# Performance work log

Hardware: AMD Instinct MI355X
Metric: run time of the kernel (lower is better)

Reference implementation:

```python
import jax, jax.numpy as jnp
import numpy as np

N_HEAD = 12
N_EMBD = 768

def setup_inputs() -> dict:
    key = jax.random.key(0)
    k1, k2, k3 = jax.random.split(key, 3)
    B, T, C = 4, 2048, N_EMBD
    x = jax.random.normal(k1, (B, T, C), dtype=jnp.float32)
    w_attn = jax.random.normal(k2, (C, 3 * C), dtype=jnp.float32) * (C ** -0.5)
    b_attn = jnp.zeros((3 * C,), dtype=jnp.float32)
    w_proj = jax.random.normal(k3, (C, C), dtype=jnp.float32) * (C ** -0.5)
    b_proj = jnp.zeros((C,), dtype=jnp.float32)
    return {"x": x, "w_attn": w_attn, "b_attn": b_attn, "w_proj": w_proj, "b_proj": b_proj}

def reference(x, w_attn, b_attn, w_proj, b_proj):
    B, T, C = x.shape
    H = N_HEAD
    D = C // H
    qkv = x @ w_attn + b_attn  # [B,T,3C]
    q, k, v = jnp.split(qkv, 3, axis=-1)
    # [B,H,T,D]
    q = q.reshape(B, T, H, D).transpose(0, 2, 1, 3)
    k = k.reshape(B, T, H, D).transpose(0, 2, 1, 3)
    v = v.reshape(B, T, H, D).transpose(0, 2, 1, 3)
    # NOTE: source scales by n_embd**-0.5, not head_dim**-0.5
    scores = jnp.einsum('bhqd,bhkd->bhqk', q, k) * (C ** -0.5)
    causal = jnp.triu(jnp.ones((T, T), dtype=bool), k=1)  # True above diagonal
    scores = jnp.where(causal, -jnp.inf, scores)
    attn = jax.nn.softmax(scores, axis=-1)
    out = jnp.einsum('bhqk,bhkd->bhqd', attn, v)  # [B,H,T,D]
    out = out.transpose(0, 2, 1, 3).reshape(B, T, C)
    return out @ w_proj + b_proj
```

## Files before the change

### kernel.cpp

```cpp
#include <hip/hip_runtime.h>
#include <cstdint>
#include <cstddef>

typedef __attribute__((ext_vector_type(8))) short bf8_t;
typedef __attribute__((ext_vector_type(4))) float f4_t;
typedef __attribute__((ext_vector_type(16))) float f16v_t;
typedef __attribute__((ext_vector_type(2))) unsigned u2_t;
typedef __attribute__((ext_vector_type(4))) unsigned u4_t;

#define DEVFN static __device__ __forceinline__
#define MFMA16(a, b, c) __builtin_amdgcn_mfma_f32_16x16x32_bf16(a, b, c, 0, 0, 0)
#define MFMA32(a, b, c) __builtin_amdgcn_mfma_f32_32x32x16_bf16(a, b, c, 0, 0, 0)

constexpr float kQscale = 0.05205877317700523f;

DEVFN short f2bs(float f) {
  uint32_t u = __builtin_bit_cast(uint32_t, f);
  u = (u + 0x7FFFu + ((u >> 16) & 1u)) >> 16;
  return (short)(uint16_t)u;
}

DEVFN unsigned cvtpk(float lo, float hi) {
  unsigned r;
  asm("v_cvt_pk_bf16_f32 %0, %1, %2" : "=v"(r) : "v"(lo), "v"(hi));
  return r;
}

DEVFN float red2_sum(float v) { return v + __shfl_xor(v, 32, 64); }

DEVFN void gload16(const void* g, void* l) {
  __builtin_amdgcn_global_load_lds(
      (const __attribute__((address_space(1))) void*)g,
      (__attribute__((address_space(3))) void*)l, 16, 0, 0);
}

__global__ __launch_bounds__(256) void prep(const float* __restrict__ x,
                                            short* __restrict__ xb,
                                            const float* __restrict__ w_attn,
                                            short* __restrict__ wat,
                                            const float* __restrict__ w_proj,
                                            short* __restrict__ wpt) {
  __shared__ float tile[32][33];
  const int blk = blockIdx.x, tid = threadIdx.x;
  if (blk < 3072) {
    const int i = blk * 256 + tid;
    const f4_t* p = (const f4_t*)x + (size_t)i * 2;
    f4_t a = p[0], b = p[1];
    bf8_t h;
    h[0] = f2bs(a[0]); h[1] = f2bs(a[1]); h[2] = f2bs(a[2]); h[3] = f2bs(a[3]);
    h[4] = f2bs(b[0]); h[5] = f2bs(b[1]); h[6] = f2bs(b[2]); h[7] = f2bs(b[3]);
    *((bf8_t*)xb + i) = h;
    return;
  }
  const float* w;
  short* wT;
  int N, n0, k0;
  if (blk < 4800) {
    const int bb = blk - 3072;
    w = w_attn; wT = wat; N = 2304;
    n0 = (bb % 72) << 5; k0 = (bb / 72) << 5;
  } else {
    const int bb = blk - 4800;
    w = w_proj; wT = wpt; N = 768;
    n0 = (bb % 24) << 5; k0 = (bb / 24) << 5;
  }
  const int tx = tid & 31, ty = tid >> 5;
#pragma unroll
  for (int i = 0; i < 4; ++i)
    tile[ty * 4 + i][tx] = w[(size_t)(k0 + ty * 4 + i) * N + n0 + tx];
  __syncthreads();
#pragma unroll
  for (int i = 0; i < 4; ++i)
    wT[(size_t)(n0 + ty * 4 + i) * 768 + k0 + tx] = f2bs(tile[tx][ty * 4 + i]);
}

template <int EPI>
__global__ __launch_bounds__(256) void gemm_bf16(
    const short* __restrict__ A, const short* __restrict__ Bt,
    const float* __restrict__ bias, float* __restrict__ outF,
    short* __restrict__ qb, short* __restrict__ kb, short* __restrict__ vtb,
    int Mdim, int Ndim, int Kdim) {
  __shared__ char smem[65536];
  const int nbx = gridDim.x;
  const int bid = blockIdx.x + nbx * blockIdx.y;
  const int xcd = bid & 7, slot = bid >> 3;
  const int mp = xcd + ((slot / nbx) << 3);
  const int np = slot % nbx;
  const int m0 = mp << 7, n0 = np << 7;
  const int tid = threadIdx.x;
  const int lane = tid & 63, wid = tid >> 6;
  const int wr = wid >> 1, wc = wid & 1;
  const int g = lane >> 4, cl = lane & 15;
  const int ldb = Kdim << 1;

  f4_t acc[4][4];
#pragma unroll
  for (int mi = 0; mi < 4; ++mi)
#pragma unroll
    for (int ni = 0; ni < 4; ++ni) acc[mi][ni] = (f4_t){0.f, 0.f, 0.f, 0.f};

  const char* ga = (const char*)(A + (size_t)m0 * Kdim);
  const char* gb = (const char*)(Bt + (size_t)n0 * Kdim);
  auto stage = [&](int b, int ks) {
    const int k0b = ks << 7;
    char* Ab = smem + (b << 14);
    char* Bb = smem + 32768 + (b << 14);
#pragma unroll
    for (int i = 0; i < 4; ++i) {
      const int doff = (wid << 12) + (i << 10);
      const int boff = doff + lane * 16;
      const int row = boff >> 7;
      const int src = row * ldb + k0b + ((boff & 127) ^ ((row & 7) << 4));
      gload16(ga + src, Ab + doff);
      gload16(gb + src, Bb + doff);
    }
  };

  const int nk = Kdim >> 6;
  stage(0, 0);
  __syncthreads();

  int cur = 0;
  for (int ks = 0; ks < nk; ++ks) {
    const int ksn = (ks + 1 < nk) ? ks + 1 : ks;
    stage(cur ^ 1, ksn);
    const char* Ab = smem + (cur << 14);
    const char* Bb = smem + 32768 + (cur << 14);
#pragma unroll
    for (int kk = 0; kk < 2; ++kk) {
      bf8_t af[4], bfv[4];
#pragma unroll
      for (int mi = 0; mi < 4; ++mi) {
        int lrow = (wr << 6) + (mi << 4) + cl;
        af[mi] = *(const bf8_t*)&Ab[(lrow << 7) + ((((kk << 2) + g) ^ (lrow & 7)) << 4)];
      }
#pragma unroll
      for (int ni = 0; ni < 4; ++ni) {
        int lrow = (wc << 6) + (ni << 4) + cl;
        bfv[ni] = *(const bf8_t*)&Bb[(lrow << 7) + ((((kk << 2) + g) ^ (lrow & 7)) << 4)];
      }
#pragma unroll
      for (int mi = 0; mi < 4; ++mi)
#pragma unroll
        for (int ni = 0; ni < 4; ++ni)
          acc[mi][ni] = MFMA16(af[mi], bfv[ni], acc[mi][ni]);
    }
    __syncthreads();
    cur ^= 1;
  }

  if constexpr (EPI == 1) {
#pragma unroll
    for (int ni = 0; ni < 4; ++ni) {
      const int n = n0 + (wc << 6) + (ni << 4) + cl;
      const float bv = bias[n];
#pragma unroll
      for (int mi = 0; mi < 4; ++mi)
#pragma unroll
        for (int r = 0; r < 4; ++r) {
          const int m = m0 + (wr << 6) + (mi << 4) + (g << 2) + r;
          outF[(size_t)m * 768 + n] = acc[mi][ni][r] + bv;
        }
    }
  } else {
    short* T = (short*)smem;
    const int sec = n0 / 768;
    const float qs = (sec == 0) ? kQscale : 1.0f;
#pragma unroll
    for (int ni = 0; ni < 4; ++ni) {
      const float bv = bias[n0 + (wc << 6) + (ni << 4) + cl];
      const int colT = (wc << 6) + (ni << 4) + cl;
#pragma unroll
      for (int mi = 0; mi < 4; ++mi)
#pragma unroll
        for (int r = 0; r < 4; ++r) {
          const int row = (wr << 6) + (mi << 4) + (g << 2) + r;
          T[row * 132 + colT] = f2bs((acc[mi][ni][r] + bv) * qs);
        }
    }
    __syncthreads();
    if (sec < 2) {
      short* dst0 = (sec == 0) ? qb : kb;
      const int tl = tid & 127, hh2 = tid >> 7;
      const int m = m0 + tl, b = m >> 11, t = m & 2047;
      const int hh = ((n0 - sec * 768) >> 6) + hh2;
      short* dst = dst0 + (size_t)(b * 12 + hh) * 131072 + (size_t)t * 64;
      const short* src = T + tl * 132 + hh2 * 64;
#pragma unroll
      for (int j = 0; j < 8; ++j)
        *(bf8_t*)(dst + j * 8) = *(const bf8_t*)(src + j * 8);
    } else {
      const int chunk = tid & 15;
      const int m = m0 + (chunk << 3);
      const int b = m >> 11, t = m & 2047;
#pragma unroll
      for (int c8 = 0; c8 < 8; ++c8) {
        const int dl = (tid >> 4) + (c8 << 4);
        const int nloc = n0 - 1536 + dl;
        const int hh = nloc >> 6, d = nloc & 63;
        bf8_t tmp;
#pragma unroll
        for (int j = 0; j < 8; ++j)
          tmp[j] = T[((chunk << 3) + j) * 132 + dl];
        *(bf8_t*)(vtb + (size_t)(b * 12 + hh) * 131072 + (size_t)d * 2048 + t) = tmp;
      }
    }
  }
}

__global__ __launch_bounds__(256, 2) void attn_fwd(const short* __restrict__ Q,
                                                   const short* __restrict__ K,
                                                   const short* __restrict__ Vt,
                                                   short* __restrict__ O) {
  __shared__ char kv_lds[2][32768];
  const int tid = threadIdx.x;
  const int lane = tid & 63, wid = tid >> 6;
  const int blk = blockIdx.x;
  const int bh = blk % 48;
  const int qg = 15 - blk / 48;
  const int qt = (qg << 2) + wid;
  const int q0 = qt << 5;
  const int col = lane & 31, hi = lane >> 5;

  const short* Qb = Q + (size_t)bh * 131072;
  const short* Kb = K + (size_t)bh * 131072;
  const short* Vb = Vt + (size_t)bh * 131072;

  bf8_t qf[4];
#pragma unroll
  for (int dc = 0; dc < 4; ++dc)
    qf[dc] = *(const bf8_t*)(Qb + (size_t)(q0 + col) * 64 + dc * 16 + hi * 8);

  const f16v_t zf = {0.f,0.f,0.f,0.f,0.f,0.f,0.f,0.f,0.f,0.f,0.f,0.f,0.f,0.f,0.f,0.f};
  f16v_t o0 = zf, o1 = zf;
  float ls[4] = {0.f, 0.f, 0.f, 0.f};

  const int nt = qg + 1;
  const int kxor = (col & 7) << 4;

  auto stage = [&](int b, int kcs) {
    char* buf = &kv_lds[b][0];
    if (wid < 2) {
      const char* g = (const char*)(Kb + (size_t)kcs * 64);
#pragma unroll
      for (int i = 0; i < 8; ++i) {
        const int doff = (wid << 13) + (i << 10);
        const int boff = doff + lane * 16;
        const int src = boff ^ (((boff >> 7) & 7) << 4);
        gload16(g + src, buf + doff);
      }
    } else {
      const char* g = (const char*)Vb + (size_t)kcs * 2;
#pragma unroll
      for (int i = 0; i < 8; ++i) {
        const int doff = ((wid - 2) << 13) + (i << 10);
        const int boff = doff + lane * 16;
        const int row = boff >> 8;
        const int src = row * 4096 + ((boff & 255) ^ ((row & 7) << 4));
        gload16(g + src, buf + 16384 + doff);
      }
    }
  };

  stage(0, 0);
  __syncthreads();

  int cur = 0;
  for (int st = 0; st < nt; ++st) {
    int kcn = (st + 1) << 7;
    if (kcn > 1920) kcn = 1920;
    stage(cur ^ 1, kcn);

#pragma unroll
    for (int h = 0; h < 2; ++h) {
      const int kc = (st << 7) + (h << 6);
      if (kc < q0 + 32) {
        const char* Kl = &kv_lds[cur][h << 13];
        const char* Vl = &kv_lds[cur][16384];
        f16v_t s0 = zf, s1 = zf;
#pragma unroll
        for (int dc = 0; dc < 4; ++dc) {
          const int fo = (dc * 32 + hi * 16) ^ kxor;
          bf8_t k0 = *(const bf8_t*)(Kl + col * 128 + fo);
          bf8_t k1 = *(const bf8_t*)(Kl + (32 + col) * 128 + fo);
          __builtin_amdgcn_s_setprio(1);
          s0 = MFMA32(k0, qf[dc], s0);
          s1 = MFMA32(k1, qf[dc], s1);
          __builtin_amdgcn_s_setprio(0);
        }
        if (kc + 63 > q0) {
          const int qq = q0 + col;
#pragma unroll
          for (int r = 0; r < 16; ++r) {
            const int kb_ = kc + (r & 3) + 8 * (r >> 2) + 4 * hi;
            if (kb_ > qq) s0[r] = -1e30f;
            if (kb_ + 32 > qq) s1[r] = -1e30f;
          }
        }
#pragma unroll
        for (int r = 0; r < 16; ++r) {
          s0[r] = __builtin_amdgcn_exp2f(s0[r]);
          s1[r] = __builtin_amdgcn_exp2f(s1[r]);
        }
#pragma unroll
        for (int r = 0; r < 4; ++r)
          ls[r] += ((s0[r] + s0[r + 4]) + (s0[r + 8] + s0[r + 12])) +
                   ((s1[r] + s1[r + 4]) + (s1[r + 8] + s1[r + 12]));
#pragma unroll
        for (int c = 0; c < 4; ++c) {
          const int b8 = (c & 1) * 8;
          float p0, p1, p2, p3, p4, p5, p6, p7;
          if (c < 2) {
            p0 = s0[b8+0]; p1 = s0[b8+1]; p2 = s0[b8+2]; p3 = s0[b8+3];
            p4 = s0[b8+4]; p5 = s0[b8+5]; p6 = s0[b8+6]; p7 = s0[b8+7];
          } else {
            p0 = s1[b8+0]; p1 = s1[b8+1]; p2 = s1[b8+2]; p3 = s1[b8+3];
            p4 = s1[b8+4]; p5 = s1[b8+5]; p6 = s1[b8+6]; p7 = s1[b8+7];
          }
          unsigned w0 = cvtpk(p0, p1), w1 = cvtpk(p2, p3);
          unsigned w2 = cvtpk(p4, p5), w3 = cvtpk(p6, p7);
          unsigned x0 = (unsigned)__shfl_xor((int)w0, 32, 64);
          unsigned x1 = (unsigned)__shfl_xor((int)w1, 32, 64);
          unsigned x2 = (unsigned)__shfl_xor((int)w2, 32, 64);
          unsigned x3 = (unsigned)__shfl_xor((int)w3, 32, 64);
          unsigned T0 = hi ? x2 : w0;
          unsigned T1 = hi ? x3 : w1;
          unsigned T2 = hi ? w2 : x0;
          unsigned T3 = hi ? w3 : x1;
          const bf8_t pf = __builtin_bit_cast(bf8_t, (u4_t){T0, T1, T2, T3});
          const int vo = ((h << 7) + c * 32 + hi * 16) ^ kxor;
          bf8_t v0 = *(const bf8_t*)(Vl + col * 256 + vo);
          bf8_t v1 = *(const bf8_t*)(Vl + (32 + col) * 256 + vo);
          __builtin_amdgcn_s_setprio(1);
          o0 = MFMA32(v0, pf, o0);
          o1 = MFMA32(v1, pf, o1);
          __builtin_amdgcn_s_setprio(0);
        }
      }
    }
    __syncthreads();
    cur ^= 1;
  }

  const float l = red2_sum((ls[0] + ls[1]) + (ls[2] + ls[3]));
  const float rl = 1.0f / l;
  const int b_ = bh / 12, hh = bh % 12;
  short* Op = O + (size_t)b_ * 2048 * 768 + (size_t)(q0 + col) * 768 + hh * 64;
#pragma unroll
  for (int rq = 0; rq < 4; ++rq) {
    u2_t w0, w1;
    w0[0] = cvtpk(o0[4*rq+0] * rl, o0[4*rq+1] * rl);
    w0[1] = cvtpk(o0[4*rq+2] * rl, o0[4*rq+3] * rl);
    w1[0] = cvtpk(o1[4*rq+0] * rl, o1[4*rq+1] * rl);
    w1[1] = cvtpk(o1[4*rq+2] * rl, o1[4*rq+3] * rl);
    *(u2_t*)(Op + rq * 8 + hi * 4) = w0;
    *(u2_t*)(Op + 32 + rq * 8 + hi * 4) = w1;
  }
}

extern "C" void kernel_launch(void* const* d_in, const int* in_sizes, int n_in,
                              void* d_out, int out_size, void* d_ws, size_t ws_size,
                              hipStream_t stream) {
  const float* x      = (const float*)d_in[0];
  const float* w_attn = (const float*)d_in[1];
  const float* b_attn = (const float*)d_in[2];
  const float* w_proj = (const float*)d_in[3];
  const float* b_proj = (const float*)d_in[4];
  float* out = (float*)d_out;

  const size_t QSZ = (size_t)4 * 12 * 2048 * 64;
  short* ws  = (short*)d_ws;
  short* qb  = ws;
  short* kb  = qb + QSZ;
  short* vtb = kb + QSZ;
  short* xb  = vtb + QSZ;
  short* ob  = xb;
  short* wat = xb + QSZ;
  short* wpt = wat + (size_t)2304 * 768;

  prep<<<5376, 256, 0, stream>>>(x, xb, w_attn, wat, w_proj, wpt);

  gemm_bf16<0><<<dim3(18, 64), 256, 0, stream>>>(xb, wat, b_attn, nullptr,
                                                 qb, kb, vtb, 8192, 2304, 768);
  attn_fwd<<<768, 256, 0, stream>>>(qb, kb, vtb, ob);
  gemm_bf16<1><<<dim3(6, 64), 256, 0, stream>>>(ob, wpt, b_proj, out,
                                                nullptr, nullptr, nullptr, 8192, 768, 768);
}
```

Measured before the change: 132.1 us.

## Single-buffer attention LDS with register staging; narrow proj GEMM tile

The attention kernel drops its double-buffered LDS (64KB) for a single 32KB buffer. The next K/V chunk is prefetched into registers during compute and written to LDS between two barriers, which halves LDS use and may allow more resident blocks, at the cost of an extra barrier and more registers. The GEMM is templated on the N tile width. The output projection now uses 64-wide tiles with twice as many blocks, to fill the GPU better on the small 768-wide GEMM.

```diff
diff --git a/kernel.cpp b/kernel.cpp
--- a/kernel.cpp
+++ b/kernel.cpp
@@ -74,37 +74,39 @@
     wT[(size_t)(n0 + ty * 4 + i) * 768 + k0 + tx] = f2bs(tile[tx][ty * 4 + i]);
 }
 
-template <int EPI>
+template <int EPI, int BN>
 __global__ __launch_bounds__(256) void gemm_bf16(
     const short* __restrict__ A, const short* __restrict__ Bt,
     const float* __restrict__ bias, float* __restrict__ outF,
     short* __restrict__ qb, short* __restrict__ kb, short* __restrict__ vtb,
     int Mdim, int Ndim, int Kdim) {
-  __shared__ char smem[65536];
+  constexpr int NI = BN / 32;
+  constexpr int BCH = BN / 32;
+  __shared__ char smem[32768 + 2 * (BN << 7)];
   const int nbx = gridDim.x;
   const int bid = blockIdx.x + nbx * blockIdx.y;
   const int xcd = bid & 7, slot = bid >> 3;
   const int mp = xcd + ((slot / nbx) << 3);
   const int np = slot % nbx;
-  const int m0 = mp << 7, n0 = np << 7;
+  const int m0 = mp << 7, n0 = np * BN;
   const int tid = threadIdx.x;
   const int lane = tid & 63, wid = tid >> 6;
   const int wr = wid >> 1, wc = wid & 1;
   const int g = lane >> 4, cl = lane & 15;
   const int ldb = Kdim << 1;
 
-  f4_t acc[4][4];
+  f4_t acc[4][NI];
 #pragma unroll
   for (int mi = 0; mi < 4; ++mi)
 #pragma unroll
-    for (int ni = 0; ni < 4; ++ni) acc[mi][ni] = (f4_t){0.f, 0.f, 0.f, 0.f};
+    for (int ni = 0; ni < NI; ++ni) acc[mi][ni] = (f4_t){0.f, 0.f, 0.f, 0.f};
 
   const char* ga = (const char*)(A + (size_t)m0 * Kdim);
   const char* gb = (const char*)(Bt + (size_t)n0 * Kdim);
   auto stage = [&](int b, int ks) {
     const int k0b = ks << 7;
     char* Ab = smem + (b << 14);
-    char* Bb = smem + 32768 + (b << 14);
+    char* Bb = smem + 32768 + b * (BN << 7);
 #pragma unroll
     for (int i = 0; i < 4; ++i) {
       const int doff = (wid << 12) + (i << 10);
@@ -112,6 +114,13 @@
       const int row = boff >> 7;
       const int src = row * ldb + k0b + ((boff & 127) ^ ((row & 7) << 4));
       gload16(ga + src, Ab + doff);
+    }
+#pragma unroll
+    for (int i = 0; i < BCH; ++i) {
+      const int doff = wid * (BN << 5) + (i << 10);
+      const int boff = doff + lane * 16;
+      const int row = boff >> 7;
+      const int src = row * ldb + k0b + ((boff & 127) ^ ((row & 7) << 4));
       gload16(gb + src, Bb + doff);
     }
   };
@@ -125,24 +134,24 @@
     const int ksn = (ks + 1 < nk) ? ks + 1 : ks;
     stage(cur ^ 1, ksn);
     const char* Ab = smem + (cur << 14);
-    const char* Bb = smem + 32768 + (cur << 14);
+    const char* Bb = smem + 32768 + cur * (BN << 7);
 #pragma unroll
     for (int kk = 0; kk < 2; ++kk) {
-      bf8_t af[4], bfv[4];
+      bf8_t af[4], bfv[NI];
 #pragma unroll
       for (int mi = 0; mi < 4; ++mi) {
         int lrow = (wr << 6) + (mi << 4) + cl;
         af[mi] = *(const bf8_t*)&Ab[(lrow << 7) + ((((kk << 2) + g) ^ (lrow & 7)) << 4)];
       }
 #pragma unroll
-      for (int ni = 0; ni < 4; ++ni) {
-        int lrow = (wc << 6) + (ni << 4) + cl;
+      for (int ni = 0; ni < NI; ++ni) {
+        int lrow = wc * (BN >> 1) + (ni << 4) + cl;
         bfv[ni] = *(const bf8_t*)&Bb[(lrow << 7) + ((((kk << 2) + g) ^ (lrow & 7)) << 4)];
       }
 #pragma unroll
       for (int mi = 0; mi < 4; ++mi)
 #pragma unroll
-        for (int ni = 0; ni < 4; ++ni)
+        for (int ni = 0; ni < NI; ++ni)
           acc[mi][ni] = MFMA16(af[mi], bfv[ni], acc[mi][ni]);
     }
     __syncthreads();
@@ -151,8 +160,8 @@
 
   if constexpr (EPI == 1) {
 #pragma unroll
-    for (int ni = 0; ni < 4; ++ni) {
-      const int n = n0 + (wc << 6) + (ni << 4) + cl;
+    for (int ni = 0; ni < NI; ++ni) {
+      const int n = n0 + wc * (BN >> 1) + (ni << 4) + cl;
       const float bv = bias[n];
 #pragma unroll
       for (int mi = 0; mi < 4; ++mi)
@@ -167,7 +176,7 @@
     const int sec = n0 / 768;
     const float qs = (sec == 0) ? kQscale : 1.0f;
 #pragma unroll
-    for (int ni = 0; ni < 4; ++ni) {
+    for (int ni = 0; ni < NI; ++ni) {
       const float bv = bias[n0 + (wc << 6) + (ni << 4) + cl];
       const int colT = (wc << 6) + (ni << 4) + cl;
 #pragma unroll
@@ -212,7 +221,7 @@
                                                    const short* __restrict__ K,
                                                    const short* __restrict__ Vt,
                                                    short* __restrict__ O) {
-  __shared__ char kv_lds[2][32768];
+  __shared__ char kv[32768];
   const int tid = threadIdx.x;
   const int lane = tid & 63, wid = tid >> 6;
   const int blk = blockIdx.x;
@@ -238,45 +247,54 @@
   const int nt = qg + 1;
   const int kxor = (col & 7) << 4;
 
-  auto stage = [&](int b, int kcs) {
-    char* buf = &kv_lds[b][0];
+  u4_t stg[8];
+  auto load_regs = [&](int kcs) {
     if (wid < 2) {
       const char* g = (const char*)(Kb + (size_t)kcs * 64);
 #pragma unroll
-      for (int i = 0; i < 8; ++i) {
-        const int doff = (wid << 13) + (i << 10);
-        const int boff = doff + lane * 16;
-        const int src = boff ^ (((boff >> 7) & 7) << 4);
-        gload16(g + src, buf + doff);
-      }
+      for (int i = 0; i < 8; ++i)
+        stg[i] = *(const u4_t*)(g + (wid << 13) + (i << 10) + lane * 16);
     } else {
       const char* g = (const char*)Vb + (size_t)kcs * 2;
 #pragma unroll
       for (int i = 0; i < 8; ++i) {
-        const int doff = ((wid - 2) << 13) + (i << 10);
-        const int boff = doff + lane * 16;
+        const int boff = ((wid - 2) << 13) + (i << 10) + lane * 16;
         const int row = boff >> 8;
-        const int src = row * 4096 + ((boff & 255) ^ ((row & 7) << 4));
-        gload16(g + src, buf + 16384 + doff);
+        stg[i] = *(const u4_t*)(g + row * 4096 + (boff & 255));
       }
     }
   };
-
-  stage(0, 0);
+  auto write_lds = [&]() {
+    if (wid < 2) {
+#pragma unroll
+      for (int i = 0; i < 8; ++i) {
+        const int boff = (wid << 13) + (i << 10) + lane * 16;
+        *(u4_t*)(kv + (boff ^ (((boff >> 7) & 7) << 4))) = stg[i];
+      }
+    } else {
+#pragma unroll
+      for (int i = 0; i < 8; ++i) {
+        const int boff = ((wid - 2) << 13) + (i << 10) + lane * 16;
+        const int row = boff >> 8;
+        *(u4_t*)(kv + 16384 + (boff & ~255) + ((boff & 255) ^ ((row & 7) << 4))) = stg[i];
+      }
+    }
+  };
+
+  load_regs(0);
+  write_lds();
   __syncthreads();
 
-  int cur = 0;
   for (int st = 0; st < nt; ++st) {
-    int kcn = (st + 1) << 7;
-    if (kcn > 1920) kcn = 1920;
-    stage(cur ^ 1, kcn);
+    const bool more = (st + 1 < nt);
+    if (more) load_regs((st + 1) << 7);
 
 #pragma unroll
     for (int h = 0; h < 2; ++h) {
       const int kc = (st << 7) + (h << 6);
       if (kc < q0 + 32) {
-        const char* Kl = &kv_lds[cur][h << 13];
-        const char* Vl = &kv_lds[cur][16384];
+        const char* Kl = kv + (h << 13);
+        const char* Vl = kv + 16384;
         f16v_t s0 = zf, s1 = zf;
 #pragma unroll
         for (int dc = 0; dc < 4; ++dc) {
@@ -338,8 +356,11 @@
         }
       }
     }
-    __syncthreads();
-    cur ^= 1;
+    if (more) {
+      __syncthreads();
+      write_lds();
+      __syncthreads();
+    }
   }
 
   const float l = red2_sum((ls[0] + ls[1]) + (ls[2] + ls[3]));
@@ -380,9 +401,9 @@
 
   prep<<<5376, 256, 0, stream>>>(x, xb, w_attn, wat, w_proj, wpt);
 
-  gemm_bf16<0><<<dim3(18, 64), 256, 0, stream>>>(xb, wat, b_attn, nullptr,
-                                                 qb, kb, vtb, 8192, 2304, 768);
+  gemm_bf16<0, 128><<<dim3(18, 64), 256, 0, stream>>>(xb, wat, b_attn, nullptr,
+                                                      qb, kb, vtb, 8192, 2304, 768);
   attn_fwd<<<768, 256, 0, stream>>>(qb, kb, vtb, ob);
-  gemm_bf16<1><<<dim3(6, 64), 256, 0, stream>>>(ob, wpt, b_proj, out,
-                                                nullptr, nullptr, nullptr, 8192, 768, 768);
-}
+  gemm_bf16<1, 64><<<dim3(12, 64), 256, 0, stream>>>(ob, wpt, b_proj, out,
+                                                     nullptr, nullptr, nullptr, 8192, 768, 768);
+}
```

Measured after the change: 129.2 us. 1.02x faster.
